# Optimization experiments

Measured on AMD Instinct MI355X. Metric: run time of the kernel, lower is better.

## Reference

```python
import jax, jax.numpy as jnp
import numpy as np

B = 65536      # batch
DIM = 32       # flow dimension
NH = 24        # hidden width of each per-dim MLP
PARITY = False # order = reversed(range(dim)) when parity is False
NEG_SLOPE = 0.2


def _causal_mask(dim, dtype):
    # mask[k, j] = 1 if j <= k ; stacked layer k corresponds to torch layer i=k+1
    # which sees x[:, :i] = columns 0..k
    return (jnp.arange(dim)[None, :] <= jnp.arange(dim - 1)[:, None]).astype(dtype)


def setup_inputs() -> dict:
    key = jax.random.key(0)
    ks = jax.random.split(key, 10)
    s = 0.1
    x = jax.random.normal(ks[0], (B, DIM), jnp.float32)
    p0 = jax.random.normal(ks[1], (2,), jnp.float32) * s          # LeafParam(2)
    W1 = jax.random.normal(ks[2], (DIM - 1, NH, DIM), jnp.float32) * s
    W1 = W1 * _causal_mask(DIM, jnp.float32)[:, None, :]          # zero padded cols j > k
    b1 = jax.random.normal(ks[3], (DIM - 1, NH), jnp.float32) * s
    W2 = jax.random.normal(ks[4], (DIM - 1, NH, NH), jnp.float32) * s
    b2 = jax.random.normal(ks[5], (DIM - 1, NH), jnp.float32) * s
    W3 = jax.random.normal(ks[6], (DIM - 1, NH, NH), jnp.float32) * s
    b3 = jax.random.normal(ks[7], (DIM - 1, NH), jnp.float32) * s
    W4 = jax.random.normal(ks[8], (DIM - 1, 2, NH), jnp.float32) * s
    b4 = jax.random.normal(ks[9], (DIM - 1, 2), jnp.float32) * s
    return {"x": x, "p0": p0, "W1": W1, "b1": b1, "W2": W2, "b2": b2,
            "W3": W3, "b3": b3, "W4": W4, "b4": b4}


def reference(x, p0, W1, b1, W2, b2, W3, b3, W4, b4):
    # SlowMAF.forward: per-dim MLP(x[:, :i]) -> (s, t); z[:, order[i]] = x[:, i]*exp(s)+t
    # All dim-1 tiny MLPs are fused into stacked batched GEMMs; the growing slice
    # x[:, :i] is realized via a causal mask on the first-layer weights (same math).
    Bsz, dim = x.shape
    lrelu = lambda h: jnp.where(h > 0, h, NEG_SLOPE * h)  # LeakyReLU(0.2)
    W1m = W1 * _causal_mask(dim, x.dtype)[:, None, :]
    h = lrelu(jnp.einsum('bd,khd->bkh', x, W1m) + b1)      # (B, dim-1, NH)
    h = lrelu(jnp.einsum('bkh,kHh->bkH', h, W2) + b2)
    h = lrelu(jnp.einsum('bkh,kHh->bkH', h, W3) + b3)
    st = jnp.einsum('bkh,koh->bko', h, W4) + b4            # (B, dim-1, 2)
    st0 = jnp.broadcast_to(p0[None, None, :], (Bsz, 1, 2)) # LeafParam for dim 0
    st_all = jnp.concatenate([st0, st], axis=1)            # (B, dim, 2)
    s = st_all[..., 0]
    t = st_all[..., 1]
    vals = x * jnp.exp(s) + t                              # (B, dim)
    order = jnp.arange(dim) if PARITY else jnp.arange(dim)[::-1]
    z = jnp.zeros_like(x).at[:, order].set(vals)
    log_det = jnp.sum(s, axis=1)                           # (B,)
    return z, log_det
```

## Files before the change

### kernel.cpp

```cpp
#include <hip/hip_runtime.h>
#include <hip/hip_bf16.h>

#define BATCH 65536
#define DIM 32
#define NEG 0.2f

typedef short    sfrag8 __attribute__((ext_vector_type(8)));
typedef float    f32x16 __attribute__((ext_vector_type(16)));
typedef unsigned u32x4  __attribute__((ext_vector_type(4)));

__device__ __forceinline__ short f2bf(float v) {
    __bf16 b = (__bf16)v;
    return __builtin_bit_cast(short, b);
}

__device__ __forceinline__ unsigned pack2bf(float v0, float v1) {
    unsigned lo = (unsigned short)f2bf(v0);
    unsigned hi = (unsigned short)f2bf(v1);
    return lo | (hi << 16);
}

__device__ float frag_elem(int k, int f, int r, int h, int j,
    const float* W1, const float* b1, const float* W2, const float* b2,
    const float* W3, const float* b3, const float* W4, const float* b4)
{
    if (f == 0) return (r < 24) ? W1[k*768 + r*32 + 8*h + j] : 0.f;
    if (f == 1) {
        if (r >= 24) return 0.f;
        int c = 16 + 8*h + j;
        if (c == 31) return b1[k*24 + r];
        return W1[k*768 + r*32 + c];
    }
    const float* W; const float* bb; int R;
    if (f < 4)      { W = W2 + k*576; bb = b2 + k*24; R = 24; }
    else if (f < 6) { W = W3 + k*576; bb = b3 + k*24; R = 24; }
    else            { W = W4 + k*48;  bb = b4 + k*2;  R = 2;  }
    if (r >= R) return 0.f;
    if ((f & 1) == 0) {
        int feat = j + 4*h + (j >= 4 ? 4 : 0);
        return W[r*24 + feat];
    } else {
        if (j < 4)            return W[r*24 + 16 + 4*h + j];
        if (j == 4 && h == 0) return bb[r];
        return 0.f;
    }
}

__global__ __launch_bounds__(256) void prep_frags(
    const float* __restrict__ W1, const float* __restrict__ b1,
    const float* __restrict__ W2, const float* __restrict__ b2,
    const float* __restrict__ W3, const float* __restrict__ b3,
    const float* __restrict__ W4, const float* __restrict__ b4,
    short* __restrict__ wsf)
{
    int t = blockIdx.x * 256 + threadIdx.x;
    int lane = t & 63, f = (t >> 6) & 7, k = t >> 9;
    int r = lane & 31, h = lane >> 5;
    sfrag8 o;
    #pragma unroll
    for (int j = 0; j < 8; j++)
        o[j] = f2bf(frag_elem(k, f, r, h, j, W1, b1, W2, b2, W3, b3, W4, b4));
    *(sfrag8*)(wsf + (size_t)t * 8) = o;
}

__device__ __forceinline__ void transition(const f32x16 a, unsigned c1,
                                           sfrag8& blo, sfrag8& bhi)
{
    unsigned P[6];
    #pragma unroll
    for (int g = 0; g < 6; g++) {
        float v0 = a[2*g], v1 = a[2*g + 1];
        v0 = fmaxf(v0, NEG * v0);
        v1 = fmaxf(v1, NEG * v1);
        P[g] = pack2bf(v0, v1);
    }
    blo = __builtin_bit_cast(sfrag8, (u32x4){P[0], P[1], P[2], P[3]});
    bhi = __builtin_bit_cast(sfrag8, (u32x4){P[4], P[5], c1, 0u});
}

template<bool PREPPED>
__global__ __launch_bounds__(256) void maf2(
    const float* __restrict__ x, const float* __restrict__ p0,
    const float* __restrict__ W1, const float* __restrict__ b1,
    const float* __restrict__ W2, const float* __restrict__ b2,
    const float* __restrict__ W3, const float* __restrict__ b3,
    const float* __restrict__ W4, const float* __restrict__ b4,
    const short* __restrict__ wsf,
    float* __restrict__ out)
{
    const int  kg   = blockIdx.y;
    const int  lane = threadIdx.x & 63;
    const int  wave = threadIdx.x >> 6;
    const bool hi   = lane >= 32;
    const int  h    = hi ? 1 : 0;
    const int  r    = lane & 31;
    const int  k0   = kg ? 4*kg - 1 : 0;
    const int  nk   = kg ? 4 : 3;
    const int  c0   = 28 - 4*kg;
    const int  colbase = (blockIdx.x * 4 + wave) * 64;
    const unsigned c1 = hi ? 0u : 0x3F80u;

    sfrag8 xlo[2], xhi[2];
    float  xa[2][4];
    #pragma unroll
    for (int t = 0; t < 2; t++) {
        const float* xp = x + (size_t)(colbase + t*32 + r) * DIM;
        float4 q0 = *(const float4*)(xp + 8*h);
        float4 q1 = *(const float4*)(xp + 8*h + 4);
        float4 q2 = *(const float4*)(xp + 16 + 8*h);
        float4 q3 = *(const float4*)(xp + 16 + 8*h + 4);
        sfrag8 lo, hh;
        lo[0]=f2bf(q0.x); lo[1]=f2bf(q0.y); lo[2]=f2bf(q0.z); lo[3]=f2bf(q0.w);
        lo[4]=f2bf(q1.x); lo[5]=f2bf(q1.y); lo[6]=f2bf(q1.z); lo[7]=f2bf(q1.w);
        hh[0]=f2bf(q2.x); hh[1]=f2bf(q2.y); hh[2]=f2bf(q2.z); hh[3]=f2bf(q2.w);
        hh[4]=f2bf(q3.x); hh[5]=f2bf(q3.y); hh[6]=f2bf(q3.z);
        hh[7] = hi ? f2bf(1.0f) : f2bf(q3.w);
        xlo[t] = lo; xhi[t] = hh;
        float4 qa = *(const float4*)(xp + 4*kg);
        xa[t][0] = qa.x; xa[t][1] = qa.y; xa[t][2] = qa.z; xa[t][3] = qa.w;
    }

    f32x16 Z;
    #pragma unroll
    for (int q = 0; q < 16; q++) Z[q] = 0.f;

    float za[2][4];
    float ld[2] = {0.f, 0.f};

    #pragma unroll
    for (int i = 0; i < 4; i++) {
        if (i < nk) {
            int k = k0 + i;
            sfrag8 F[8];
            if (PREPPED) {
                const short* fp = wsf + ((size_t)k * 512 + lane) * 8;
                #pragma unroll
                for (int f = 0; f < 8; f++) F[f] = *(const sfrag8*)(fp + f * 512);
            } else {
                #pragma unroll
                for (int f = 0; f < 8; f++)
                    #pragma unroll
                    for (int j = 0; j < 8; j++)
                        F[f][j] = f2bf(frag_elem(k, f, r, h, j,
                                                 W1, b1, W2, b2, W3, b3, W4, b4));
            }

            f32x16 acc[2];
            sfrag8 blo[2], bh2[2];
            #pragma unroll
            for (int t = 0; t < 2; t++) {
                f32x16 a = __builtin_amdgcn_mfma_f32_32x32x16_bf16(F[0], xlo[t], Z, 0, 0, 0);
                acc[t]   = __builtin_amdgcn_mfma_f32_32x32x16_bf16(F[1], xhi[t], a, 0, 0, 0);
            }
            #pragma unroll
            for (int t = 0; t < 2; t++) transition(acc[t], c1, blo[t], bh2[t]);
            #pragma unroll
            for (int t = 0; t < 2; t++) {
                f32x16 a = __builtin_amdgcn_mfma_f32_32x32x16_bf16(F[2], blo[t], Z, 0, 0, 0);
                acc[t]   = __builtin_amdgcn_mfma_f32_32x32x16_bf16(F[3], bh2[t], a, 0, 0, 0);
            }
            #pragma unroll
            for (int t = 0; t < 2; t++) transition(acc[t], c1, blo[t], bh2[t]);
            #pragma unroll
            for (int t = 0; t < 2; t++) {
                f32x16 a = __builtin_amdgcn_mfma_f32_32x32x16_bf16(F[4], blo[t], Z, 0, 0, 0);
                acc[t]   = __builtin_amdgcn_mfma_f32_32x32x16_bf16(F[5], bh2[t], a, 0, 0, 0);
            }
            #pragma unroll
            for (int t = 0; t < 2; t++) transition(acc[t], c1, blo[t], bh2[t]);
            #pragma unroll
            for (int t = 0; t < 2; t++) {
                f32x16 a = __builtin_amdgcn_mfma_f32_32x32x16_bf16(F[6], blo[t], Z, 0, 0, 0);
                acc[t]   = __builtin_amdgcn_mfma_f32_32x32x16_bf16(F[7], bh2[t], a, 0, 0, 0);
            }

            #pragma unroll
            for (int t = 0; t < 2; t++) {
                float s  = acc[t][0];
                float tt = acc[t][1];
                float e  = __expf(s);
                if (kg) { za[t][3 - i] = xa[t][i] * e + tt; }
                else if (i < 3) { za[t][2 - i] = xa[t][i + 1] * e + tt; }
                ld[t] += s;
            }
        }
    }

    if (kg == 0) {
        float s0 = p0[0], t0 = p0[1];
        float e0 = __expf(s0);
        #pragma unroll
        for (int t = 0; t < 2; t++) {
            za[t][3] = xa[t][0] * e0 + t0;
            ld[t] += s0;
        }
    }

    if (!hi) {
        #pragma unroll
        for (int t = 0; t < 2; t++) {
            int b = colbase + t*32 + r;
            float4 v; v.x = za[t][0]; v.y = za[t][1]; v.z = za[t][2]; v.w = za[t][3];
            *(float4*)(out + (size_t)b * DIM + c0) = v;
            atomicAdd(out + (size_t)BATCH * DIM + b, ld[t]);
        }
    }
}

extern "C" void kernel_launch(void* const* d_in, const int* in_sizes, int n_in,
                              void* d_out, int out_size, void* d_ws, size_t ws_size,
                              hipStream_t stream)
{
    const float* x  = (const float*)d_in[0];
    const float* p0 = (const float*)d_in[1];
    const float* W1 = (const float*)d_in[2];
    const float* b1 = (const float*)d_in[3];
    const float* W2 = (const float*)d_in[4];
    const float* b2 = (const float*)d_in[5];
    const float* W3 = (const float*)d_in[6];
    const float* b3 = (const float*)d_in[7];
    const float* W4 = (const float*)d_in[8];
    const float* b4 = (const float*)d_in[9];
    float* out = (float*)d_out;

    const size_t FRG = (size_t)31 * 8 * 64 * 8;
    if (ws_size >= FRG * sizeof(short)) {
        short* wsf = (short*)d_ws;
        prep_frags<<<62, 256, 0, stream>>>(W1, b1, W2, b2, W3, b3, W4, b4, wsf);
        maf2<true><<<dim3(256, 8), 256, 0, stream>>>(
            x, p0, W1, b1, W2, b2, W3, b3, W4, b4, wsf, out);
    } else {
        maf2<false><<<dim3(256, 8), 256, 0, stream>>>(
            x, p0, W1, b1, W2, b2, W3, b3, W4, b4, nullptr, out);
    }
}
```

Measured before the change: 115.8 us.

## Split work into per-wave tiles of 32 rows and 2 MLPs each

Reorganises the grid so each wave handles a 32-row batch tile and only two of the per-dimension MLPs, instead of two 32-row tiles and four MLPs. The goal is more parallel waves, fewer live registers (launch bounds now request 4 blocks per SM), and both weight fragment sets loaded up front. The trade-off is more redundant x loads and conversions, more atomicAdds on log_det (16 groups instead of 8), and fewer independent MFMA chains per wave to hide latency.

After: 119.1 us. 2.8% more time.

```diff
diff --git a/kernel.cpp b/kernel.cpp
--- a/kernel.cpp
+++ b/kernel.cpp
@@ -78,8 +78,30 @@
     bhi = __builtin_bit_cast(sfrag8, (u32x4){P[4], P[5], c1, 0u});
 }
 
+__device__ __forceinline__ void mlp_chain(const sfrag8* F, const sfrag8 xlo,
+                                          const sfrag8 xhi, unsigned c1,
+                                          float& s, float& tt)
+{
+    f32x16 Z;
+    #pragma unroll
+    for (int q = 0; q < 16; q++) Z[q] = 0.f;
+    sfrag8 blo, bhi;
+    f32x16 a = __builtin_amdgcn_mfma_f32_32x32x16_bf16(F[0], xlo, Z, 0, 0, 0);
+    a        = __builtin_amdgcn_mfma_f32_32x32x16_bf16(F[1], xhi, a, 0, 0, 0);
+    transition(a, c1, blo, bhi);
+    a        = __builtin_amdgcn_mfma_f32_32x32x16_bf16(F[2], blo, Z, 0, 0, 0);
+    a        = __builtin_amdgcn_mfma_f32_32x32x16_bf16(F[3], bhi, a, 0, 0, 0);
+    transition(a, c1, blo, bhi);
+    a        = __builtin_amdgcn_mfma_f32_32x32x16_bf16(F[4], blo, Z, 0, 0, 0);
+    a        = __builtin_amdgcn_mfma_f32_32x32x16_bf16(F[5], bhi, a, 0, 0, 0);
+    transition(a, c1, blo, bhi);
+    a        = __builtin_amdgcn_mfma_f32_32x32x16_bf16(F[6], blo, Z, 0, 0, 0);
+    a        = __builtin_amdgcn_mfma_f32_32x32x16_bf16(F[7], bhi, a, 0, 0, 0);
+    s = a[0]; tt = a[1];
+}
+
 template<bool PREPPED>
-__global__ __launch_bounds__(256) void maf2(
+__global__ __launch_bounds__(256, 4) void maf3(
     const float* __restrict__ x, const float* __restrict__ p0,
     const float* __restrict__ W1, const float* __restrict__ b1,
     const float* __restrict__ W2, const float* __restrict__ b2,
@@ -88,122 +110,78 @@
     const short* __restrict__ wsf,
     float* __restrict__ out)
 {
-    const int  kg   = blockIdx.y;
     const int  lane = threadIdx.x & 63;
-    const int  wave = threadIdx.x >> 6;
+    const int  wid  = (blockIdx.x << 2) + (threadIdx.x >> 6);
+    const int  tile = wid & 2047;
+    const int  kg   = wid >> 11;
     const bool hi   = lane >= 32;
     const int  h    = hi ? 1 : 0;
     const int  r    = lane & 31;
-    const int  k0   = kg ? 4*kg - 1 : 0;
-    const int  nk   = kg ? 4 : 3;
-    const int  c0   = 28 - 4*kg;
-    const int  colbase = (blockIdx.x * 4 + wave) * 64;
+    const int  k0   = kg ? 2*kg - 1 : 0;
+    const int  c0   = 30 - 2*kg;
+    const int  col  = tile * 32 + r;
     const unsigned c1 = hi ? 0u : 0x3F80u;
 
-    sfrag8 xlo[2], xhi[2];
-    float  xa[2][4];
-    #pragma unroll
-    for (int t = 0; t < 2; t++) {
-        const float* xp = x + (size_t)(colbase + t*32 + r) * DIM;
-        float4 q0 = *(const float4*)(xp + 8*h);
-        float4 q1 = *(const float4*)(xp + 8*h + 4);
-        float4 q2 = *(const float4*)(xp + 16 + 8*h);
-        float4 q3 = *(const float4*)(xp + 16 + 8*h + 4);
-        sfrag8 lo, hh;
-        lo[0]=f2bf(q0.x); lo[1]=f2bf(q0.y); lo[2]=f2bf(q0.z); lo[3]=f2bf(q0.w);
-        lo[4]=f2bf(q1.x); lo[5]=f2bf(q1.y); lo[6]=f2bf(q1.z); lo[7]=f2bf(q1.w);
-        hh[0]=f2bf(q2.x); hh[1]=f2bf(q2.y); hh[2]=f2bf(q2.z); hh[3]=f2bf(q2.w);
-        hh[4]=f2bf(q3.x); hh[5]=f2bf(q3.y); hh[6]=f2bf(q3.z);
-        hh[7] = hi ? f2bf(1.0f) : f2bf(q3.w);
-        xlo[t] = lo; xhi[t] = hh;
-        float4 qa = *(const float4*)(xp + 4*kg);
-        xa[t][0] = qa.x; xa[t][1] = qa.y; xa[t][2] = qa.z; xa[t][3] = qa.w;
-    }
-
-    f32x16 Z;
-    #pragma unroll
-    for (int q = 0; q < 16; q++) Z[q] = 0.f;
-
-    float za[2][4];
-    float ld[2] = {0.f, 0.f};
-
-    #pragma unroll
-    for (int i = 0; i < 4; i++) {
-        if (i < nk) {
-            int k = k0 + i;
-            sfrag8 F[8];
-            if (PREPPED) {
-                const short* fp = wsf + ((size_t)k * 512 + lane) * 8;
-                #pragma unroll
-                for (int f = 0; f < 8; f++) F[f] = *(const sfrag8*)(fp + f * 512);
-            } else {
-                #pragma unroll
-                for (int f = 0; f < 8; f++)
-                    #pragma unroll
-                    for (int j = 0; j < 8; j++)
-                        F[f][j] = f2bf(frag_elem(k, f, r, h, j,
-                                                 W1, b1, W2, b2, W3, b3, W4, b4));
+    const float* xp = x + (size_t)col * DIM;
+    float4 q0 = *(const float4*)(xp + 8*h);
+    float4 q1 = *(const float4*)(xp + 8*h + 4);
+    float4 q2 = *(const float4*)(xp + 16 + 8*h);
+    float4 q3 = *(const float4*)(xp + 16 + 8*h + 4);
+    float2 qa = *(const float2*)(xp + 2*kg);
+
+    sfrag8 F0[8], F1[8];
+    if (PREPPED) {
+        const short* fp0 = wsf + ((size_t)k0 * 512 + lane) * 8;
+        const short* fp1 = fp0 + 512 * 8;
+        #pragma unroll
+        for (int f = 0; f < 8; f++) F0[f] = *(const sfrag8*)(fp0 + f * 512);
+        #pragma unroll
+        for (int f = 0; f < 8; f++) F1[f] = *(const sfrag8*)(fp1 + f * 512);
+    } else {
+        #pragma unroll
+        for (int f = 0; f < 8; f++)
+            #pragma unroll
+            for (int j = 0; j < 8; j++) {
+                F0[f][j] = f2bf(frag_elem(k0, f, r, h, j,
+                                          W1, b1, W2, b2, W3, b3, W4, b4));
+                F1[f][j] = f2bf(frag_elem(k0+1, f, r, h, j,
+                                          W1, b1, W2, b2, W3, b3, W4, b4));
             }
-
-            f32x16 acc[2];
-            sfrag8 blo[2], bh2[2];
-            #pragma unroll
-            for (int t = 0; t < 2; t++) {
-                f32x16 a = __builtin_amdgcn_mfma_f32_32x32x16_bf16(F[0], xlo[t], Z, 0, 0, 0);
-                acc[t]   = __builtin_amdgcn_mfma_f32_32x32x16_bf16(F[1], xhi[t], a, 0, 0, 0);
-            }
-            #pragma unroll
-            for (int t = 0; t < 2; t++) transition(acc[t], c1, blo[t], bh2[t]);
-            #pragma unroll
-            for (int t = 0; t < 2; t++) {
-                f32x16 a = __builtin_amdgcn_mfma_f32_32x32x16_bf16(F[2], blo[t], Z, 0, 0, 0);
-                acc[t]   = __builtin_amdgcn_mfma_f32_32x32x16_bf16(F[3], bh2[t], a, 0, 0, 0);
-            }
-            #pragma unroll
-            for (int t = 0; t < 2; t++) transition(acc[t], c1, blo[t], bh2[t]);
-            #pragma unroll
-            for (int t = 0; t < 2; t++) {
-                f32x16 a = __builtin_amdgcn_mfma_f32_32x32x16_bf16(F[4], blo[t], Z, 0, 0, 0);
-                acc[t]   = __builtin_amdgcn_mfma_f32_32x32x16_bf16(F[5], bh2[t], a, 0, 0, 0);
-            }
-            #pragma unroll
-            for (int t = 0; t < 2; t++) transition(acc[t], c1, blo[t], bh2[t]);
-            #pragma unroll
-            for (int t = 0; t < 2; t++) {
-                f32x16 a = __builtin_amdgcn_mfma_f32_32x32x16_bf16(F[6], blo[t], Z, 0, 0, 0);
-                acc[t]   = __builtin_amdgcn_mfma_f32_32x32x16_bf16(F[7], bh2[t], a, 0, 0, 0);
-            }
-
-            #pragma unroll
-            for (int t = 0; t < 2; t++) {
-                float s  = acc[t][0];
-                float tt = acc[t][1];
-                float e  = __expf(s);
-                if (kg) { za[t][3 - i] = xa[t][i] * e + tt; }
-                else if (i < 3) { za[t][2 - i] = xa[t][i + 1] * e + tt; }
-                ld[t] += s;
-            }
-        }
-    }
-
-    if (kg == 0) {
-        float s0 = p0[0], t0 = p0[1];
-        float e0 = __expf(s0);
-        #pragma unroll
-        for (int t = 0; t < 2; t++) {
-            za[t][3] = xa[t][0] * e0 + t0;
-            ld[t] += s0;
-        }
-    }
+    }
+
+    sfrag8 xlo, xhi;
+    xlo[0]=f2bf(q0.x); xlo[1]=f2bf(q0.y); xlo[2]=f2bf(q0.z); xlo[3]=f2bf(q0.w);
+    xlo[4]=f2bf(q1.x); xlo[5]=f2bf(q1.y); xlo[6]=f2bf(q1.z); xlo[7]=f2bf(q1.w);
+    xhi[0]=f2bf(q2.x); xhi[1]=f2bf(q2.y); xhi[2]=f2bf(q2.z); xhi[3]=f2bf(q2.w);
+    xhi[4]=f2bf(q3.x); xhi[5]=f2bf(q3.y); xhi[6]=f2bf(q3.z);
+    xhi[7] = hi ? f2bf(1.0f) : f2bf(q3.w);
+
+    float s0c, t0c;
+    mlp_chain(F0, xlo, xhi, c1, s0c, t0c);
+    float e0c = __expf(s0c);
+    float xv0 = kg ? qa.x : qa.y;
+    float r0  = fmaf(xv0, e0c, t0c);
+    float sum_s = s0c;
+
+    float r1 = 0.f;
+    if (kg) {
+        float s1c, t1c;
+        mlp_chain(F1, xlo, xhi, c1, s1c, t1c);
+        r1 = fmaf(qa.y, __expf(s1c), t1c);
+        sum_s += s1c;
+    }
+
+    float ps = p0[0], pt = p0[1];
+    float leaf = fmaf(qa.x, __expf(ps), pt);
+
+    float zax = kg ? r1 : r0;
+    float zay = kg ? r0 : leaf;
+    if (!kg) sum_s += ps;
 
     if (!hi) {
-        #pragma unroll
-        for (int t = 0; t < 2; t++) {
-            int b = colbase + t*32 + r;
-            float4 v; v.x = za[t][0]; v.y = za[t][1]; v.z = za[t][2]; v.w = za[t][3];
-            *(float4*)(out + (size_t)b * DIM + c0) = v;
-            atomicAdd(out + (size_t)BATCH * DIM + b, ld[t]);
-        }
+        float2 v; v.x = zax; v.y = zay;
+        *(float2*)(out + (size_t)col * DIM + c0) = v;
+        atomicAdd(out + (size_t)BATCH * DIM + col, sum_s);
     }
 }
 
@@ -227,10 +205,10 @@
     if (ws_size >= FRG * sizeof(short)) {
         short* wsf = (short*)d_ws;
         prep_frags<<<62, 256, 0, stream>>>(W1, b1, W2, b2, W3, b3, W4, b4, wsf);
-        maf2<true><<<dim3(256, 8), 256, 0, stream>>>(
+        maf3<true><<<8192, 256, 0, stream>>>(
             x, p0, W1, b1, W2, b2, W3, b3, W4, b4, wsf, out);
     } else {
-        maf2<false><<<dim3(256, 8), 256, 0, stream>>>(
+        maf3<false><<<8192, 256, 0, stream>>>(
             x, p0, W1, b1, W2, b2, W3, b3, W4, b4, nullptr, out);
     }
 }
```

## Assign one MLP index per wave to expose more parallelism

Applied to the files above, without the earlier changes.

Remaps the grid so each wave computes a single per-dimension MLP for a 64-row tile, instead of four sequential MLPs. Weight fragments are loaded once up front, and outputs are written as scalars with one atomic log-det add per k. The intent is to shorten each wave's serial MFMA chains and increase occupancy. The trade-off is reading x about 31 times instead of 8, plus roughly four times more atomics and scattered scalar stores. The bf16 packing is also switched to a paired conversion intrinsic.

After: 132.4 us. 1.14x slower.

```diff
diff --git a/kernel.cpp b/kernel.cpp
--- a/kernel.cpp
+++ b/kernel.cpp
@@ -7,6 +7,7 @@
 
 typedef short    sfrag8 __attribute__((ext_vector_type(8)));
 typedef float    f32x16 __attribute__((ext_vector_type(16)));
+typedef float    f32x2  __attribute__((ext_vector_type(2)));
 typedef unsigned u32x4  __attribute__((ext_vector_type(4)));
 
 __device__ __forceinline__ short f2bf(float v) {
@@ -14,10 +15,10 @@
     return __builtin_bit_cast(short, b);
 }
 
-__device__ __forceinline__ unsigned pack2bf(float v0, float v1) {
-    unsigned lo = (unsigned short)f2bf(v0);
-    unsigned hi = (unsigned short)f2bf(v1);
-    return lo | (hi << 16);
+__device__ __forceinline__ unsigned pk2(float a, float b) {
+    __hip_bfloat162 h2 = __float22bfloat162_rn(float2{a, b});
+    unsigned u; __builtin_memcpy(&u, &h2, 4);
+    return u;
 }
 
 __device__ float frag_elem(int k, int f, int r, int h, int j,
@@ -69,17 +70,16 @@
     unsigned P[6];
     #pragma unroll
     for (int g = 0; g < 6; g++) {
-        float v0 = a[2*g], v1 = a[2*g + 1];
-        v0 = fmaxf(v0, NEG * v0);
-        v1 = fmaxf(v1, NEG * v1);
-        P[g] = pack2bf(v0, v1);
+        f32x2 v = {a[2*g], a[2*g + 1]};
+        f32x2 m = __builtin_elementwise_max(v, v * NEG);
+        P[g] = pk2(m.x, m.y);
     }
     blo = __builtin_bit_cast(sfrag8, (u32x4){P[0], P[1], P[2], P[3]});
     bhi = __builtin_bit_cast(sfrag8, (u32x4){P[4], P[5], c1, 0u});
 }
 
 template<bool PREPPED>
-__global__ __launch_bounds__(256) void maf2(
+__global__ __launch_bounds__(256) void maf4(
     const float* __restrict__ x, const float* __restrict__ p0,
     const float* __restrict__ W1, const float* __restrict__ b1,
     const float* __restrict__ W2, const float* __restrict__ b2,
@@ -88,20 +88,33 @@
     const short* __restrict__ wsf,
     float* __restrict__ out)
 {
-    const int  kg   = blockIdx.y;
     const int  lane = threadIdx.x & 63;
-    const int  wave = threadIdx.x >> 6;
+    const int  wid  = (blockIdx.x << 2) + (threadIdx.x >> 6);
+    const int  tile = wid & 1023;
+    const int  k    = wid >> 10;
     const bool hi   = lane >= 32;
     const int  h    = hi ? 1 : 0;
     const int  r    = lane & 31;
-    const int  k0   = kg ? 4*kg - 1 : 0;
-    const int  nk   = kg ? 4 : 3;
-    const int  c0   = 28 - 4*kg;
-    const int  colbase = (blockIdx.x * 4 + wave) * 64;
+    const int  c0   = 30 - k;
+    const int  colbase = tile * 64;
     const unsigned c1 = hi ? 0u : 0x3F80u;
 
+    sfrag8 F[8];
+    if (PREPPED) {
+        const short* fp = wsf + ((size_t)k * 512 + lane) * 8;
+        #pragma unroll
+        for (int f = 0; f < 8; f++) F[f] = *(const sfrag8*)(fp + f * 512);
+    } else {
+        #pragma unroll
+        for (int f = 0; f < 8; f++)
+            #pragma unroll
+            for (int j = 0; j < 8; j++)
+                F[f][j] = f2bf(frag_elem(k, f, r, h, j,
+                                         W1, b1, W2, b2, W3, b3, W4, b4));
+    }
+
     sfrag8 xlo[2], xhi[2];
-    float  xa[2][4];
+    float  xv[2], x0[2];
     #pragma unroll
     for (int t = 0; t < 2; t++) {
         const float* xp = x + (size_t)(colbase + t*32 + r) * DIM;
@@ -109,100 +122,64 @@
         float4 q1 = *(const float4*)(xp + 8*h + 4);
         float4 q2 = *(const float4*)(xp + 16 + 8*h);
         float4 q3 = *(const float4*)(xp + 16 + 8*h + 4);
-        sfrag8 lo, hh;
-        lo[0]=f2bf(q0.x); lo[1]=f2bf(q0.y); lo[2]=f2bf(q0.z); lo[3]=f2bf(q0.w);
-        lo[4]=f2bf(q1.x); lo[5]=f2bf(q1.y); lo[6]=f2bf(q1.z); lo[7]=f2bf(q1.w);
-        hh[0]=f2bf(q2.x); hh[1]=f2bf(q2.y); hh[2]=f2bf(q2.z); hh[3]=f2bf(q2.w);
-        hh[4]=f2bf(q3.x); hh[5]=f2bf(q3.y); hh[6]=f2bf(q3.z);
-        hh[7] = hi ? f2bf(1.0f) : f2bf(q3.w);
-        xlo[t] = lo; xhi[t] = hh;
-        float4 qa = *(const float4*)(xp + 4*kg);
-        xa[t][0] = qa.x; xa[t][1] = qa.y; xa[t][2] = qa.z; xa[t][3] = qa.w;
+        float last = hi ? 1.0f : q3.w;
+        xlo[t] = __builtin_bit_cast(sfrag8, (u32x4){
+            pk2(q0.x, q0.y), pk2(q0.z, q0.w), pk2(q1.x, q1.y), pk2(q1.z, q1.w)});
+        xhi[t] = __builtin_bit_cast(sfrag8, (u32x4){
+            pk2(q2.x, q2.y), pk2(q2.z, q2.w), pk2(q3.x, q3.y), pk2(q3.z, last)});
+        xv[t] = xp[k + 1];
+        x0[t] = xp[0];
     }
 
     f32x16 Z;
     #pragma unroll
     for (int q = 0; q < 16; q++) Z[q] = 0.f;
 
-    float za[2][4];
-    float ld[2] = {0.f, 0.f};
-
-    #pragma unroll
-    for (int i = 0; i < 4; i++) {
-        if (i < nk) {
-            int k = k0 + i;
-            sfrag8 F[8];
-            if (PREPPED) {
-                const short* fp = wsf + ((size_t)k * 512 + lane) * 8;
-                #pragma unroll
-                for (int f = 0; f < 8; f++) F[f] = *(const sfrag8*)(fp + f * 512);
-            } else {
-                #pragma unroll
-                for (int f = 0; f < 8; f++)
-                    #pragma unroll
-                    for (int j = 0; j < 8; j++)
-                        F[f][j] = f2bf(frag_elem(k, f, r, h, j,
-                                                 W1, b1, W2, b2, W3, b3, W4, b4));
-            }
-
-            f32x16 acc[2];
-            sfrag8 blo[2], bh2[2];
-            #pragma unroll
-            for (int t = 0; t < 2; t++) {
-                f32x16 a = __builtin_amdgcn_mfma_f32_32x32x16_bf16(F[0], xlo[t], Z, 0, 0, 0);
-                acc[t]   = __builtin_amdgcn_mfma_f32_32x32x16_bf16(F[1], xhi[t], a, 0, 0, 0);
-            }
-            #pragma unroll
-            for (int t = 0; t < 2; t++) transition(acc[t], c1, blo[t], bh2[t]);
-            #pragma unroll
-            for (int t = 0; t < 2; t++) {
-                f32x16 a = __builtin_amdgcn_mfma_f32_32x32x16_bf16(F[2], blo[t], Z, 0, 0, 0);
-                acc[t]   = __builtin_amdgcn_mfma_f32_32x32x16_bf16(F[3], bh2[t], a, 0, 0, 0);
-            }
-            #pragma unroll
-            for (int t = 0; t < 2; t++) transition(acc[t], c1, blo[t], bh2[t]);
-            #pragma unroll
-            for (int t = 0; t < 2; t++) {
-                f32x16 a = __builtin_amdgcn_mfma_f32_32x32x16_bf16(F[4], blo[t], Z, 0, 0, 0);
-                acc[t]   = __builtin_amdgcn_mfma_f32_32x32x16_bf16(F[5], bh2[t], a, 0, 0, 0);
-            }
-            #pragma unroll
-            for (int t = 0; t < 2; t++) transition(acc[t], c1, blo[t], bh2[t]);
-            #pragma unroll
-            for (int t = 0; t < 2; t++) {
-                f32x16 a = __builtin_amdgcn_mfma_f32_32x32x16_bf16(F[6], blo[t], Z, 0, 0, 0);
-                acc[t]   = __builtin_amdgcn_mfma_f32_32x32x16_bf16(F[7], bh2[t], a, 0, 0, 0);
-            }
-
-            #pragma unroll
-            for (int t = 0; t < 2; t++) {
-                float s  = acc[t][0];
-                float tt = acc[t][1];
-                float e  = __expf(s);
-                if (kg) { za[t][3 - i] = xa[t][i] * e + tt; }
-                else if (i < 3) { za[t][2 - i] = xa[t][i + 1] * e + tt; }
-                ld[t] += s;
-            }
-        }
-    }
-
-    if (kg == 0) {
-        float s0 = p0[0], t0 = p0[1];
-        float e0 = __expf(s0);
+    f32x16 acc[2];
+    sfrag8 blo[2], bh2[2];
+
+    #pragma unroll
+    for (int t = 0; t < 2; t++) {
+        f32x16 a = __builtin_amdgcn_mfma_f32_32x32x16_bf16(F[0], xlo[t], Z, 0, 0, 0);
+        acc[t]   = __builtin_amdgcn_mfma_f32_32x32x16_bf16(F[1], xhi[t], a, 0, 0, 0);
+    }
+    #pragma unroll
+    for (int t = 0; t < 2; t++) transition(acc[t], c1, blo[t], bh2[t]);
+    #pragma unroll
+    for (int t = 0; t < 2; t++) {
+        f32x16 a = __builtin_amdgcn_mfma_f32_32x32x16_bf16(F[2], blo[t], Z, 0, 0, 0);
+        acc[t]   = __builtin_amdgcn_mfma_f32_32x32x16_bf16(F[3], bh2[t], a, 0, 0, 0);
+    }
+    #pragma unroll
+    for (int t = 0; t < 2; t++) transition(acc[t], c1, blo[t], bh2[t]);
+    #pragma unroll
+    for (int t = 0; t < 2; t++) {
+        f32x16 a = __builtin_amdgcn_mfma_f32_32x32x16_bf16(F[4], blo[t], Z, 0, 0, 0);
+        acc[t]   = __builtin_amdgcn_mfma_f32_32x32x16_bf16(F[5], bh2[t], a, 0, 0, 0);
+    }
+    #pragma unroll
+    for (int t = 0; t < 2; t++) transition(acc[t], c1, blo[t], bh2[t]);
+    #pragma unroll
+    for (int t = 0; t < 2; t++) {
+        f32x16 a = __builtin_amdgcn_mfma_f32_32x32x16_bf16(F[6], blo[t], Z, 0, 0, 0);
+        acc[t]   = __builtin_amdgcn_mfma_f32_32x32x16_bf16(F[7], bh2[t], a, 0, 0, 0);
+    }
+
+    if (!hi) {
+        float ps = p0[0], pt = p0[1];
         #pragma unroll
         for (int t = 0; t < 2; t++) {
-            za[t][3] = xa[t][0] * e0 + t0;
-            ld[t] += s0;
-        }
-    }
-
-    if (!hi) {
-        #pragma unroll
-        for (int t = 0; t < 2; t++) {
-            int b = colbase + t*32 + r;
-            float4 v; v.x = za[t][0]; v.y = za[t][1]; v.z = za[t][2]; v.w = za[t][3];
-            *(float4*)(out + (size_t)b * DIM + c0) = v;
-            atomicAdd(out + (size_t)BATCH * DIM + b, ld[t]);
+            int   col = colbase + t*32 + r;
+            float s   = acc[t][0];
+            float tt  = acc[t][1];
+            float z   = fmaf(xv[t], __expf(s), tt);
+            out[(size_t)col * DIM + c0] = z;
+            float ld = s;
+            if (k == 0) {
+                out[(size_t)col * DIM + 31] = fmaf(x0[t], __expf(ps), pt);
+                ld += ps;
+            }
+            atomicAdd(out + (size_t)BATCH * DIM + col, ld);
         }
     }
 }
@@ -227,10 +204,10 @@
     if (ws_size >= FRG * sizeof(short)) {
         short* wsf = (short*)d_ws;
         prep_frags<<<62, 256, 0, stream>>>(W1, b1, W2, b2, W3, b3, W4, b4, wsf);
-        maf2<true><<<dim3(256, 8), 256, 0, stream>>>(
+        maf4<true><<<7936, 256, 0, stream>>>(
             x, p0, W1, b1, W2, b2, W3, b3, W4, b4, wsf, out);
     } else {
-        maf2<false><<<dim3(256, 8), 256, 0, stream>>>(
+        maf4<false><<<7936, 256, 0, stream>>>(
             x, p0, W1, b1, W2, b2, W3, b3, W4, b4, nullptr, out);
     }
 }
```

## Split MAF into bf16 pre-pack, MFMA phase with LDS weights, and epilogue kernel

Applied to the files above, without the earlier changes.

Restructures the pipeline into four kernels. One pre-converts x to packed bf16, one builds the weight fragments, and an MFMA phase stages each group's weight fragments in shared memory and writes (s,t) pairs to a workspace buffer. A final elementwise kernel applies the affine transform and reduces log_det with wave shuffles, which replaces the global atomicAdd and its dependence on a zeroed output. The bf16 conversion and transition also switch to packed intrinsics. The cost is two extra launches plus about 16 MB of extra workspace traffic for the intermediate (s,t) values.

New measurement: 119.7 us. 3.3% more time.

```diff
diff --git a/kernel.cpp b/kernel.cpp
--- a/kernel.cpp
+++ b/kernel.cpp
@@ -7,6 +7,7 @@
 
 typedef short    sfrag8 __attribute__((ext_vector_type(8)));
 typedef float    f32x16 __attribute__((ext_vector_type(16)));
+typedef float    f32x2  __attribute__((ext_vector_type(2)));
 typedef unsigned u32x4  __attribute__((ext_vector_type(4)));
 
 __device__ __forceinline__ short f2bf(float v) {
@@ -14,10 +15,10 @@
     return __builtin_bit_cast(short, b);
 }
 
-__device__ __forceinline__ unsigned pack2bf(float v0, float v1) {
-    unsigned lo = (unsigned short)f2bf(v0);
-    unsigned hi = (unsigned short)f2bf(v1);
-    return lo | (hi << 16);
+__device__ __forceinline__ unsigned pk2(float a, float b) {
+    __hip_bfloat162 h2 = __float22bfloat162_rn(float2{a, b});
+    unsigned u; __builtin_memcpy(&u, &h2, 4);
+    return u;
 }
 
 __device__ float frag_elem(int k, int f, int r, int h, int j,
@@ -63,29 +64,155 @@
     *(sfrag8*)(wsf + (size_t)t * 8) = o;
 }
 
+__global__ __launch_bounds__(256) void prep_xQ(const float* __restrict__ x,
+                                               unsigned* __restrict__ xQ)
+{
+    int t = blockIdx.x * 256 + threadIdx.x;
+    int b = t >> 4, p = t & 15;
+    float v0 = x[(size_t)b * DIM + 2*p];
+    float v1 = (p == 15) ? 1.0f : x[(size_t)b * DIM + 2*p + 1];
+    xQ[t] = pk2(v0, v1);
+}
+
 __device__ __forceinline__ void transition(const f32x16 a, unsigned c1,
                                            sfrag8& blo, sfrag8& bhi)
 {
     unsigned P[6];
     #pragma unroll
     for (int g = 0; g < 6; g++) {
-        float v0 = a[2*g], v1 = a[2*g + 1];
-        v0 = fmaxf(v0, NEG * v0);
-        v1 = fmaxf(v1, NEG * v1);
-        P[g] = pack2bf(v0, v1);
+        f32x2 v = {a[2*g], a[2*g + 1]};
+        f32x2 m = __builtin_elementwise_max(v, v * NEG);
+        P[g] = pk2(m.x, m.y);
     }
     blo = __builtin_bit_cast(sfrag8, (u32x4){P[0], P[1], P[2], P[3]});
     bhi = __builtin_bit_cast(sfrag8, (u32x4){P[4], P[5], c1, 0u});
 }
 
-template<bool PREPPED>
-__global__ __launch_bounds__(256) void maf2(
+__global__ __launch_bounds__(256) void phaseA(
+    const unsigned* __restrict__ xQ, const short* __restrict__ wsf,
+    float2* __restrict__ stST)
+{
+    __shared__ __align__(16) short lds[4 * 8 * 64 * 8];
+    const int tid  = threadIdx.x;
+    const int lane = tid & 63;
+    const int wave = tid >> 6;
+    const int kg   = blockIdx.y;
+    const int k0   = kg ? 4*kg - 1 : 0;
+    const int nk   = kg ? 4 : 3;
+
+    {
+        const short* src = wsf + (size_t)k0 * 4096;
+        #pragma unroll
+        for (int it = 0; it < 8; it++) {
+            int off = it * 2048 + tid * 8;
+            *(sfrag8*)(lds + off) = *(const sfrag8*)(src + off);
+        }
+    }
+    __syncthreads();
+
+    const bool hi = lane >= 32;
+    const int  h  = hi ? 1 : 0;
+    const int  r  = lane & 31;
+    const unsigned c1 = hi ? 0u : 0x3F80u;
+    const int  colbase = (blockIdx.x * 4 + wave) * 64;
+
+    sfrag8 xlo[2], xhi[2];
+    #pragma unroll
+    for (int t = 0; t < 2; t++) {
+        const unsigned* xq = xQ + (size_t)(colbase + t*32 + r) * 16;
+        xlo[t] = __builtin_bit_cast(sfrag8, *(const u32x4*)(xq + 4*h));
+        xhi[t] = __builtin_bit_cast(sfrag8, *(const u32x4*)(xq + 8 + 4*h));
+    }
+
+    f32x16 Z;
+    #pragma unroll
+    for (int q = 0; q < 16; q++) Z[q] = 0.f;
+
+    #pragma unroll
+    for (int i = 0; i < 4; i++) {
+        if (i < nk) {
+            const short* fb = lds + i * 4096;
+            sfrag8 F[8];
+            #pragma unroll
+            for (int f = 0; f < 8; f++)
+                F[f] = *(const sfrag8*)(fb + f * 512 + lane * 8);
+
+            f32x16 acc[2];
+            sfrag8 blo[2], bh2[2];
+            #pragma unroll
+            for (int t = 0; t < 2; t++) {
+                f32x16 a = __builtin_amdgcn_mfma_f32_32x32x16_bf16(F[0], xlo[t], Z, 0, 0, 0);
+                acc[t]   = __builtin_amdgcn_mfma_f32_32x32x16_bf16(F[1], xhi[t], a, 0, 0, 0);
+            }
+            #pragma unroll
+            for (int t = 0; t < 2; t++) transition(acc[t], c1, blo[t], bh2[t]);
+            #pragma unroll
+            for (int t = 0; t < 2; t++) {
+                f32x16 a = __builtin_amdgcn_mfma_f32_32x32x16_bf16(F[2], blo[t], Z, 0, 0, 0);
+                acc[t]   = __builtin_amdgcn_mfma_f32_32x32x16_bf16(F[3], bh2[t], a, 0, 0, 0);
+            }
+            #pragma unroll
+            for (int t = 0; t < 2; t++) transition(acc[t], c1, blo[t], bh2[t]);
+            #pragma unroll
+            for (int t = 0; t < 2; t++) {
+                f32x16 a = __builtin_amdgcn_mfma_f32_32x32x16_bf16(F[4], blo[t], Z, 0, 0, 0);
+                acc[t]   = __builtin_amdgcn_mfma_f32_32x32x16_bf16(F[5], bh2[t], a, 0, 0, 0);
+            }
+            #pragma unroll
+            for (int t = 0; t < 2; t++) transition(acc[t], c1, blo[t], bh2[t]);
+            #pragma unroll
+            for (int t = 0; t < 2; t++) {
+                f32x16 a = __builtin_amdgcn_mfma_f32_32x32x16_bf16(F[6], blo[t], Z, 0, 0, 0);
+                acc[t]   = __builtin_amdgcn_mfma_f32_32x32x16_bf16(F[7], bh2[t], a, 0, 0, 0);
+            }
+
+            if (!hi) {
+                #pragma unroll
+                for (int t = 0; t < 2; t++) {
+                    int col = colbase + t*32 + r;
+                    stST[(size_t)(k0 + i) * BATCH + col] =
+                        float2{acc[t][0], acc[t][1]};
+                }
+            }
+        }
+    }
+}
+
+__global__ __launch_bounds__(256) void phaseB(
+    const float* __restrict__ x, const float* __restrict__ p0,
+    const float2* __restrict__ stST, float* __restrict__ out)
+{
+    int t = blockIdx.x * 256 + threadIdx.x;
+    int b = t >> 3, q = t & 7;
+    float4 xm = *(const float4*)(x + (size_t)b * DIM + (28 - 4*q));
+    float xmv[4] = {xm.w, xm.z, xm.y, xm.x};
+    float ps = p0[0], pt = p0[1];
+    float zz[4];
+    float ld = 0.f;
+    #pragma unroll
+    for (int i = 0; i < 4; i++) {
+        int c = 4*q + i;
+        if (c < 31) {
+            float2 st = stST[(size_t)(30 - c) * BATCH + b];
+            zz[i] = fmaf(xmv[i], __expf(st.x), st.y);
+            ld += st.x;
+        } else {
+            zz[i] = fmaf(xmv[i], __expf(ps), pt);
+        }
+    }
+    *(float4*)(out + (size_t)b * DIM + 4*q) = float4{zz[0], zz[1], zz[2], zz[3]};
+    ld += __shfl_xor(ld, 1, 64);
+    ld += __shfl_xor(ld, 2, 64);
+    ld += __shfl_xor(ld, 4, 64);
+    if (q == 0) out[(size_t)BATCH * DIM + b] = ld + ps;
+}
+
+__global__ __launch_bounds__(256) void maf_fb(
     const float* __restrict__ x, const float* __restrict__ p0,
     const float* __restrict__ W1, const float* __restrict__ b1,
     const float* __restrict__ W2, const float* __restrict__ b2,
     const float* __restrict__ W3, const float* __restrict__ b3,
     const float* __restrict__ W4, const float* __restrict__ b4,
-    const short* __restrict__ wsf,
     float* __restrict__ out)
 {
     const int  kg   = blockIdx.y;
@@ -109,13 +236,11 @@
         float4 q1 = *(const float4*)(xp + 8*h + 4);
         float4 q2 = *(const float4*)(xp + 16 + 8*h);
         float4 q3 = *(const float4*)(xp + 16 + 8*h + 4);
-        sfrag8 lo, hh;
-        lo[0]=f2bf(q0.x); lo[1]=f2bf(q0.y); lo[2]=f2bf(q0.z); lo[3]=f2bf(q0.w);
-        lo[4]=f2bf(q1.x); lo[5]=f2bf(q1.y); lo[6]=f2bf(q1.z); lo[7]=f2bf(q1.w);
-        hh[0]=f2bf(q2.x); hh[1]=f2bf(q2.y); hh[2]=f2bf(q2.z); hh[3]=f2bf(q2.w);
-        hh[4]=f2bf(q3.x); hh[5]=f2bf(q3.y); hh[6]=f2bf(q3.z);
-        hh[7] = hi ? f2bf(1.0f) : f2bf(q3.w);
-        xlo[t] = lo; xhi[t] = hh;
+        float last = hi ? 1.0f : q3.w;
+        xlo[t] = __builtin_bit_cast(sfrag8, (u32x4){
+            pk2(q0.x, q0.y), pk2(q0.z, q0.w), pk2(q1.x, q1.y), pk2(q1.z, q1.w)});
+        xhi[t] = __builtin_bit_cast(sfrag8, (u32x4){
+            pk2(q2.x, q2.y), pk2(q2.z, q2.w), pk2(q3.x, q3.y), pk2(q3.z, last)});
         float4 qa = *(const float4*)(xp + 4*kg);
         xa[t][0] = qa.x; xa[t][1] = qa.y; xa[t][2] = qa.z; xa[t][3] = qa.w;
     }
@@ -132,19 +257,12 @@
         if (i < nk) {
             int k = k0 + i;
             sfrag8 F[8];
-            if (PREPPED) {
-                const short* fp = wsf + ((size_t)k * 512 + lane) * 8;
+            #pragma unroll
+            for (int f = 0; f < 8; f++)
                 #pragma unroll
-                for (int f = 0; f < 8; f++) F[f] = *(const sfrag8*)(fp + f * 512);
-            } else {
-                #pragma unroll
-                for (int f = 0; f < 8; f++)
-                    #pragma unroll
-                    for (int j = 0; j < 8; j++)
-                        F[f][j] = f2bf(frag_elem(k, f, r, h, j,
-                                                 W1, b1, W2, b2, W3, b3, W4, b4));
-            }
-
+                for (int j = 0; j < 8; j++)
+                    F[f][j] = f2bf(frag_elem(k, f, r, h, j,
+                                             W1, b1, W2, b2, W3, b3, W4, b4));
             f32x16 acc[2];
             sfrag8 blo[2], bh2[2];
             #pragma unroll
@@ -173,14 +291,13 @@
                 f32x16 a = __builtin_amdgcn_mfma_f32_32x32x16_bf16(F[6], blo[t], Z, 0, 0, 0);
                 acc[t]   = __builtin_amdgcn_mfma_f32_32x32x16_bf16(F[7], bh2[t], a, 0, 0, 0);
             }
-
             #pragma unroll
             for (int t = 0; t < 2; t++) {
                 float s  = acc[t][0];
                 float tt = acc[t][1];
                 float e  = __expf(s);
-                if (kg) { za[t][3 - i] = xa[t][i] * e + tt; }
-                else if (i < 3) { za[t][2 - i] = xa[t][i + 1] * e + tt; }
+                if (kg) { za[t][3 - i] = fmaf(xa[t][i], e, tt); }
+                else if (i < 3) { za[t][2 - i] = fmaf(xa[t][i + 1], e, tt); }
                 ld[t] += s;
             }
         }
@@ -191,7 +308,7 @@
         float e0 = __expf(s0);
         #pragma unroll
         for (int t = 0; t < 2; t++) {
-            za[t][3] = xa[t][0] * e0 + t0;
+            za[t][3] = fmaf(xa[t][0], e0, t0);
             ld[t] += s0;
         }
     }
@@ -223,14 +340,21 @@
     const float* b4 = (const float*)d_in[9];
     float* out = (float*)d_out;
 
-    const size_t FRG = (size_t)31 * 8 * 64 * 8;
-    if (ws_size >= FRG * sizeof(short)) {
-        short* wsf = (short*)d_ws;
+    const size_t XQ_OFF  = 0;
+    const size_t FRG_OFF = 4194304;
+    const size_t ST_OFF  = 4456448;
+    const size_t WS_NEED = ST_OFF + (size_t)31 * BATCH * 8;
+
+    if (ws_size >= WS_NEED) {
+        unsigned* xQ   = (unsigned*)((char*)d_ws + XQ_OFF);
+        short*    wsf  = (short*)((char*)d_ws + FRG_OFF);
+        float2*   stST = (float2*)((char*)d_ws + ST_OFF);
+        prep_xQ<<<BATCH * 16 / 256, 256, 0, stream>>>(x, xQ);
         prep_frags<<<62, 256, 0, stream>>>(W1, b1, W2, b2, W3, b3, W4, b4, wsf);
-        maf2<true><<<dim3(256, 8), 256, 0, stream>>>(
-            x, p0, W1, b1, W2, b2, W3, b3, W4, b4, wsf, out);
+        phaseA<<<dim3(256, 8), 256, 0, stream>>>(xQ, wsf, stST);
+        phaseB<<<BATCH * 8 / 256, 256, 0, stream>>>(x, p0, stST, out);
     } else {
-        maf2<false><<<dim3(256, 8), 256, 0, stream>>>(
-            x, p0, W1, b1, W2, b2, W3, b3, W4, b4, nullptr, out);
-    }
-}
+        maf_fb<<<dim3(256, 8), 256, 0, stream>>>(
+            x, p0, W1, b1, W2, b2, W3, b3, W4, b4, out);
+    }
+}
```
